# Kernel optimization log

Measured on AMD Instinct MI355X. Metric: run time of the kernel, lower is better.

## Reference

```python
import jax, jax.numpy as jnp
import numpy as np

N, K, C, H, V = 4096, 32, 128, 128, 21   # residues, kNN, node/edge dim, hidden, vocab
NEG_SLOPE = 0.2

def gatv2(src_feat, tgt_feat, edge_feat, Wl, bl, Wr, br, We, be, att, b_out):
    # GATv2Conv (1 head, eval mode) on a regular kNN graph.
    # src_feat: [N,K,Din] gathered source-node features per edge; tgt_feat: [N,Din]
    xl = src_feat @ Wl + bl                       # [N,K,C]
    xr = tgt_feat @ Wr + br                       # [N,C]
    ee = edge_feat @ We + be                      # [N,K,C]
    m = jax.nn.leaky_relu(xl + xr[:, None, :] + ee, NEG_SLOPE)
    alpha = jax.nn.softmax(jnp.einsum('nkc,c->nk', m, att), axis=1)
    return jnp.einsum('nk,nkc->nc', alpha, xl) + b_out

def setup_inputs():
    key = jax.random.key(0)
    ks = jax.random.split(key, 32)
    w = lambda k, s: jax.random.normal(k, s, jnp.float32) * 0.05
    z0 = lambda s: jnp.zeros(s, jnp.float32)
    return dict(
        E=jax.random.normal(ks[0], (N, K, C), jnp.float32),
        E_idx=jax.random.randint(ks[1], (N, K), 0, N),
        S=jax.random.randint(ks[2], (N,), 0, V),
        mask=jnp.ones((N,), jnp.float32),
        chain_M=jnp.ones((N,), jnp.float32),
        z=jax.random.normal(ks[3], (N,), jnp.float32),
        Wl1=w(ks[4], (C, C)), bl1=z0((C,)),
        Wr1=w(ks[5], (C, C)), br1=z0((C,)),
        We1=w(ks[6], (C, C)), be1=z0((C,)),
        a1=w(ks[7], (C,)), bo1=z0((C,)),
        Wl2=w(ks[8], (C + H, C)), bl2=z0((C,)),
        Wr2=w(ks[9], (C + H, C)), br2=z0((C,)),
        We2=w(ks[10], (C, C)), be2=z0((C,)),
        a2=w(ks[11], (C,)), bo2=z0((C,)),
        W_s=w(ks[12], (V, H)),
        W_out=w(ks[13], (C, V)), b_out=z0((V,)),
    )

def reference(E, E_idx, S, mask, chain_M, z,
              Wl1, bl1, Wr1, br1, We1, be1, a1, bo1,
              Wl2, bl2, Wr2, br2, We2, be2, a2, bo2,
              W_s, W_out, b_out):
    # encoder GAT over zero-initialized node features
    x0 = jnp.zeros((N, C), E.dtype)
    node_attr = gatv2(x0[E_idx], x0, E, Wl1, bl1, Wr1, br1, We1, be1, a1, bo1)
    seq_attr = W_s[S]                                        # [N,H]
    h_full = jnp.concatenate([node_attr, seq_attr], -1)      # [N,C+H]
    h_mask = jnp.concatenate([node_attr, jnp.zeros_like(seq_attr)], -1)
    cm = chain_M * mask
    decoding_order = jnp.argsort((cm + 1e-4) * jnp.abs(z))   # [N]
    P = jax.nn.one_hot(decoding_order, N, dtype=E.dtype)     # [N,N] permutation
    L = 1.0 - jnp.triu(jnp.ones((N, N), E.dtype))            # strictly lower tri
    order_mask_backward = jnp.einsum('ij,iq,jp->qp', L, P, P)
    mask_attend = jnp.take_along_axis(order_mask_backward, E_idx, axis=1)[..., None]
    m1d = mask[:, None, None]
    mask_bw = m1d * mask_attend
    mask_fw = m1d * (1.0 - mask_attend)
    # per-edge source features: neighbor seq embedding visible only if decoded earlier
    src = h_full[E_idx] * mask_bw + h_mask[E_idx] * mask_fw  # [N,K,C+H]
    out = gatv2(src, h_mask, E, Wl2, bl2, Wr2, br2, We2, be2, a2, bo2)
    logits = out @ W_out + b_out
    return jax.nn.log_softmax(logits, axis=-1)
```

## Files before the change

kernel.cpp:

```cpp
#include <hip/hip_runtime.h>
#include <hip/hip_bf16.h>

typedef short short8 __attribute__((ext_vector_type(8)));
typedef float float4v __attribute__((ext_vector_type(4)));

#define WS_T   0
#define WS_D   2688
#define WS_C   2816
#define WS_O   2944
#define WS_A2  3072
#define WS_KEY 3200

__device__ __forceinline__ unsigned int pack2bf(float a, float b) {
  union { float f; unsigned int u; } xa, xb;
  xa.f = a; xb.f = b;
  return ((xa.u + 0x8000u) >> 16) | ((xb.u + 0x8000u) & 0xFFFF0000u);
}

__global__ __launch_bounds__(256) void pg7_pre(
    const float* __restrict__ Wl2, const float* __restrict__ Wr2,
    const float* __restrict__ We2, const float* __restrict__ bl1,
    const float* __restrict__ bl2, const float* __restrict__ br2,
    const float* __restrict__ be2, const float* __restrict__ a2,
    const float* __restrict__ bo1, const float* __restrict__ bo2,
    const float* __restrict__ W_s, const float* __restrict__ mask,
    const float* __restrict__ chain_M, const float* __restrict__ z,
    void* __restrict__ ws)
{
  short* wsW = (short*)ws;
  float* F = (float*)ws + 8192;
  const int b = blockIdx.x, tid = threadIdx.x;
  if (b == 0) {
    for (int s = tid; s < 16384; s += 256) {
      const int row = s >> 7, c = s & 127;
      const int q = row >> 5, lh = (row & 31) >> 3, j = row & 7;
      const int t = c >> 4, cl = c & 15;
      union { float f; unsigned int u; } x; x.f = We2[s];
      const unsigned int r = x.u + 0x7FFFu + ((x.u >> 16) & 1u);
      wsW[(((q * 8 + t) * 64) + lh * 16 + cl) * 8 + j] = (short)(r >> 16);
    }
    if (tid < 128) {
      const int c = tid;
      float cl0 = 0.f, cr0 = 0.f;
      for (int i = 0; i < 128; i++) {
        const float s = bl1[i] + bo1[i];
        cl0 += s * Wl2[i * 128 + c];
        cr0 += s * Wr2[i * 128 + c];
      }
      F[WS_D + c]  = be2[c] + bl2[c] + br2[c] + cr0;
      F[WS_C + c]  = cl0;
      F[WS_O + c]  = bl2[c] + bo2[c];
      F[WS_A2 + c] = a2[c];
    }
  } else if (b <= 21) {
    const int v = b - 1;
    if (tid < 128) {
      const int c = tid;
      float acc = 0.f;
      for (int h = 0; h < 128; h++)
        acc += W_s[v * 128 + h] * Wl2[(128 + h) * 128 + c];
      F[WS_T + v * 128 + c] = acc;
    }
  } else {
    const int n = (b - 22) * 256 + tid;
    F[WS_KEY + n] = (chain_M[n] * mask[n] + 1e-4f) * fabsf(z[n]);
  }
}

__global__ __launch_bounds__(256) void pg7_main(
    const float* __restrict__ E, const int* __restrict__ E_idx,
    const int* __restrict__ S, const float* __restrict__ mask,
    const float* __restrict__ W_out, const float* __restrict__ b_out,
    const void* __restrict__ ws, float* __restrict__ out)
{
  __shared__ float ldsout[4][128];
  __shared__ float ldswk[4][32];
  __shared__ int   ldsrv[4][32];

  const short* wsW = (const short*)ws;
  const float* F = (const float*)ws + 8192;
  const int tid  = threadIdx.x;
  const int wave = tid >> 6;
  const int lane = tid & 63;
  const int quad = lane >> 4;
  const int lid  = lane & 15;
  const int n    = blockIdx.x * 4 + wave;
  const float maskn = mask[n];

  if (lane < 32) {
    const int j = E_idx[n * 32 + lane];
    const float keyn = F[WS_KEY + n], kj = F[WS_KEY + j];
    const int before = (kj < keyn) || (kj == keyn && j < n);
    ldswk[wave][lane] = before ? maskn : 0.f;
    ldsrv[wave][lane] = S[j] * 128;
  }
  __builtin_amdgcn_wave_barrier();

  short8 afr[2][4];
#pragma unroll
  for (int g = 0; g < 2; g++) {
    const float* erow = E + (size_t)(n * 32 + g * 16 + lid) * 128 + quad * 8;
#pragma unroll
    for (int q = 0; q < 4; q++) {
      const float4 A = *(const float4*)(erow + q * 32);
      const float4 B = *(const float4*)(erow + q * 32 + 4);
      union { short8 s; unsigned int u[4]; } v;
      v.u[0] = pack2bf(A.x, A.y);
      v.u[1] = pack2bf(A.z, A.w);
      v.u[2] = pack2bf(B.x, B.y);
      v.u[3] = pack2bf(B.z, B.w);
      afr[g][q] = v.s;
    }
  }

  int rows[2][4]; float wks[2][4];
#pragma unroll
  for (int g = 0; g < 2; g++)
#pragma unroll
    for (int r = 0; r < 4; r++) {
      const int kk = g * 16 + quad * 4 + r;
      rows[g][r] = ldsrv[wave][kk];
      wks[g][r]  = ldswk[wave][kk];
    }

  float part[2][4] = {{0.f, 0.f, 0.f, 0.f}, {0.f, 0.f, 0.f, 0.f}};
#pragma unroll
  for (int t = 0; t < 8; t++) {
    short8 bfr[4];
#pragma unroll
    for (int q = 0; q < 4; q++)
      bfr[q] = *(const short8*)(wsW + (((q * 8 + t) * 64) + lane) * 8);
    float4v ac0 = {0.f, 0.f, 0.f, 0.f}, ac1 = {0.f, 0.f, 0.f, 0.f};
#pragma unroll
    for (int q = 0; q < 4; q++) {
      ac0 = __builtin_amdgcn_mfma_f32_16x16x32_bf16(afr[0][q], bfr[q], ac0, 0, 0, 0);
      ac1 = __builtin_amdgcn_mfma_f32_16x16x32_bf16(afr[1][q], bfr[q], ac1, 0, 0, 0);
    }
    const int c = t * 16 + lid;
    const float dvt  = F[WS_D + c] + maskn * F[WS_C + c];
    const float a2vt = F[WS_A2 + c];
#pragma unroll
    for (int r = 0; r < 4; r++) {
      float v0 = ac0[r] + dvt + wks[0][r] * F[WS_T + rows[0][r] + c];
      float v1 = ac1[r] + dvt + wks[1][r] * F[WS_T + rows[1][r] + c];
      v0 = fmaxf(v0, 0.f) + 0.2f * fminf(v0, 0.f);
      v1 = fmaxf(v1, 0.f) + 0.2f * fminf(v1, 0.f);
      part[0][r] = fmaf(v0, a2vt, part[0][r]);
      part[1][r] = fmaf(v1, a2vt, part[1][r]);
    }
  }
  float sreg[2][4];
#pragma unroll
  for (int g = 0; g < 2; g++)
#pragma unroll
    for (int r = 0; r < 4; r++) {
      float v = part[g][r];
      v += __shfl_xor(v, 1);
      v += __shfl_xor(v, 2);
      v += __shfl_xor(v, 4);
      v += __shfl_xor(v, 8);
      sreg[g][r] = v;
    }

  float mx = -1e30f;
#pragma unroll
  for (int g = 0; g < 2; g++)
#pragma unroll
    for (int r = 0; r < 4; r++) mx = fmaxf(mx, sreg[g][r]);
  mx = fmaxf(mx, __shfl_xor(mx, 16));
  mx = fmaxf(mx, __shfl_xor(mx, 32));
  float eg[2][4], esum = 0.f;
#pragma unroll
  for (int g = 0; g < 2; g++)
#pragma unroll
    for (int r = 0; r < 4; r++) {
      eg[g][r] = expf(sreg[g][r] - mx);
      esum += eg[g][r];
    }
  esum += __shfl_xor(esum, 16);
  esum += __shfl_xor(esum, 32);
  const float inv = 1.f / esum;
  float cg[2][4];
#pragma unroll
  for (int g = 0; g < 2; g++)
#pragma unroll
    for (int r = 0; r < 4; r++) cg[g][r] = eg[g][r] * inv * wks[g][r];

  float o0 = F[WS_O + lane]      + maskn * F[WS_C + lane];
  float o1 = F[WS_O + lane + 64] + maskn * F[WS_C + lane + 64];
#pragma unroll
  for (int kk = 0; kk < 32; kk++) {
    const int g = kk >> 4, sq = (kk >> 2) & 3, r = kk & 3;
    const float cf = __shfl(cg[g][r], sq * 16);
    const int row = ldsrv[wave][kk];
    o0 = fmaf(cf, F[WS_T + row + lane], o0);
    o1 = fmaf(cf, F[WS_T + row + lane + 64], o1);
  }
  ldsout[wave][lane]      = o0;
  ldsout[wave][lane + 64] = o1;
  __builtin_amdgcn_wave_barrier();

  float l0 = 0.f, l1 = 0.f, l2 = 0.f, l3 = 0.f;
  if (lane < 21) {
    const float* wo = W_out + lane;
#pragma unroll 8
    for (int c = 0; c < 128; c += 4) {
      l0 = fmaf(ldsout[wave][c],     wo[c * 21],       l0);
      l1 = fmaf(ldsout[wave][c + 1], wo[(c + 1) * 21], l1);
      l2 = fmaf(ldsout[wave][c + 2], wo[(c + 2) * 21], l2);
      l3 = fmaf(ldsout[wave][c + 3], wo[(c + 3) * 21], l3);
    }
  }
  float lg = (lane < 21) ? (b_out[lane] + ((l0 + l1) + (l2 + l3))) : -1e30f;
  float lmx = lg;
  lmx = fmaxf(lmx, __shfl_xor(lmx, 1));
  lmx = fmaxf(lmx, __shfl_xor(lmx, 2));
  lmx = fmaxf(lmx, __shfl_xor(lmx, 4));
  lmx = fmaxf(lmx, __shfl_xor(lmx, 8));
  lmx = fmaxf(lmx, __shfl_xor(lmx, 16));
  float ex = (lane < 21) ? expf(lg - lmx) : 0.f;
  float es = ex;
  es += __shfl_xor(es, 1);
  es += __shfl_xor(es, 2);
  es += __shfl_xor(es, 4);
  es += __shfl_xor(es, 8);
  es += __shfl_xor(es, 16);
  if (lane < 21)
    out[n * 21 + lane] = lg - lmx - logf(es);
}

extern "C" void kernel_launch(void* const* d_in, const int* in_sizes, int n_in,
                              void* d_out, int out_size, void* d_ws, size_t ws_size,
                              hipStream_t stream)
{
  const float* E       = (const float*)d_in[0];
  const int*   E_idx   = (const int*)d_in[1];
  const int*   S       = (const int*)d_in[2];
  const float* mask    = (const float*)d_in[3];
  const float* chain_M = (const float*)d_in[4];
  const float* z       = (const float*)d_in[5];
  const float* bl1     = (const float*)d_in[7];
  const float* bo1     = (const float*)d_in[13];
  const float* Wl2     = (const float*)d_in[14];
  const float* bl2     = (const float*)d_in[15];
  const float* Wr2     = (const float*)d_in[16];
  const float* br2     = (const float*)d_in[17];
  const float* We2     = (const float*)d_in[18];
  const float* be2     = (const float*)d_in[19];
  const float* a2      = (const float*)d_in[20];
  const float* bo2     = (const float*)d_in[21];
  const float* W_s     = (const float*)d_in[22];
  const float* W_out   = (const float*)d_in[23];
  const float* b_out   = (const float*)d_in[24];

  pg7_pre<<<38, 256, 0, stream>>>(Wl2, Wr2, We2, bl1, bl2, br2, be2, a2,
                                  bo1, bo2, W_s, mask, chain_M, z, d_ws);
  pg7_main<<<1024, 256, 0, stream>>>(E, E_idx, S, mask, W_out, b_out, d_ws,
                                     (float*)d_out);
}
```

Before: 173.0 us.

## Fold output projection into per-vocab tables to skip per-node 128-wide aggregation

```diff
diff --git a/kernel.cpp b/kernel.cpp
--- a/kernel.cpp
+++ b/kernel.cpp
@@ -10,6 +10,9 @@
 #define WS_O   2944
 #define WS_A2  3072
 #define WS_KEY 3200
+#define WS_G   7296
+#define WS_B0  7744
+#define WS_B1  7776
 
 __device__ __forceinline__ unsigned int pack2bf(float a, float b) {
   union { float f; unsigned int u; } xa, xb;
@@ -17,7 +20,7 @@
   return ((xa.u + 0x8000u) >> 16) | ((xb.u + 0x8000u) & 0xFFFF0000u);
 }
 
-__global__ __launch_bounds__(256) void pg7_pre(
+__global__ __launch_bounds__(256) void pg8_pre(
     const float* __restrict__ Wl2, const float* __restrict__ Wr2,
     const float* __restrict__ We2, const float* __restrict__ bl1,
     const float* __restrict__ bl2, const float* __restrict__ br2,
@@ -67,13 +70,38 @@
   }
 }
 
-__global__ __launch_bounds__(256) void pg7_main(
+__global__ __launch_bounds__(256) void pg8_pre2(
+    const float* __restrict__ W_out, const float* __restrict__ b_out,
+    void* __restrict__ ws)
+{
+  float* F = (float*)ws + 8192;
+  const int idx = blockIdx.x * 256 + threadIdx.x;
+  if (idx < 441) {
+    const int v = idx / 21, u = idx % 21;
+    float acc = 0.f;
+    for (int c = 0; c < 128; c++)
+      acc += F[WS_T + v * 128 + c] * W_out[c * 21 + u];
+    F[WS_G + v * 21 + u] = acc;
+  } else if (idx < 462) {
+    const int u = idx - 441;
+    float acc = b_out[u];
+    for (int c = 0; c < 128; c++)
+      acc += F[WS_O + c] * W_out[c * 21 + u];
+    F[WS_B0 + u] = acc;
+  } else if (idx < 483) {
+    const int u = idx - 462;
+    float acc = 0.f;
+    for (int c = 0; c < 128; c++)
+      acc += F[WS_C + c] * W_out[c * 21 + u];
+    F[WS_B1 + u] = acc;
+  }
+}
+
+__global__ __launch_bounds__(256, 4) void pg8_main(
     const float* __restrict__ E, const int* __restrict__ E_idx,
     const int* __restrict__ S, const float* __restrict__ mask,
-    const float* __restrict__ W_out, const float* __restrict__ b_out,
     const void* __restrict__ ws, float* __restrict__ out)
 {
-  __shared__ float ldsout[4][128];
   __shared__ float ldswk[4][32];
   __shared__ int   ldsrv[4][32];
 
@@ -92,7 +120,7 @@
     const float keyn = F[WS_KEY + n], kj = F[WS_KEY + j];
     const int before = (kj < keyn) || (kj == keyn && j < n);
     ldswk[wave][lane] = before ? maskn : 0.f;
-    ldsrv[wave][lane] = S[j] * 128;
+    ldsrv[wave][lane] = S[j];
   }
   __builtin_amdgcn_wave_barrier();
 
@@ -119,7 +147,7 @@
 #pragma unroll
     for (int r = 0; r < 4; r++) {
       const int kk = g * 16 + quad * 4 + r;
-      rows[g][r] = ldsrv[wave][kk];
+      rows[g][r] = ldsrv[wave][kk] * 128;
       wks[g][r]  = ldswk[wave][kk];
     }
 
@@ -186,32 +214,15 @@
 #pragma unroll
     for (int r = 0; r < 4; r++) cg[g][r] = eg[g][r] * inv * wks[g][r];
 
-  float o0 = F[WS_O + lane]      + maskn * F[WS_C + lane];
-  float o1 = F[WS_O + lane + 64] + maskn * F[WS_C + lane + 64];
+  float lg = (lane < 21) ? (F[WS_B0 + lane] + maskn * F[WS_B1 + lane]) : -1e30f;
 #pragma unroll
   for (int kk = 0; kk < 32; kk++) {
     const int g = kk >> 4, sq = (kk >> 2) & 3, r = kk & 3;
     const float cf = __shfl(cg[g][r], sq * 16);
-    const int row = ldsrv[wave][kk];
-    o0 = fmaf(cf, F[WS_T + row + lane], o0);
-    o1 = fmaf(cf, F[WS_T + row + lane + 64], o1);
-  }
-  ldsout[wave][lane]      = o0;
-  ldsout[wave][lane + 64] = o1;
-  __builtin_amdgcn_wave_barrier();
-
-  float l0 = 0.f, l1 = 0.f, l2 = 0.f, l3 = 0.f;
-  if (lane < 21) {
-    const float* wo = W_out + lane;
-#pragma unroll 8
-    for (int c = 0; c < 128; c += 4) {
-      l0 = fmaf(ldsout[wave][c],     wo[c * 21],       l0);
-      l1 = fmaf(ldsout[wave][c + 1], wo[(c + 1) * 21], l1);
-      l2 = fmaf(ldsout[wave][c + 2], wo[(c + 2) * 21], l2);
-      l3 = fmaf(ldsout[wave][c + 3], wo[(c + 3) * 21], l3);
-    }
-  }
-  float lg = (lane < 21) ? (b_out[lane] + ((l0 + l1) + (l2 + l3))) : -1e30f;
+    const int row = ldsrv[wave][kk] * 21;
+    if (lane < 21) lg = fmaf(cf, F[WS_G + row + lane], lg);
+  }
+
   float lmx = lg;
   lmx = fmaxf(lmx, __shfl_xor(lmx, 1));
   lmx = fmaxf(lmx, __shfl_xor(lmx, 2));
@@ -253,8 +264,8 @@
   const float* W_out   = (const float*)d_in[23];
   const float* b_out   = (const float*)d_in[24];
 
-  pg7_pre<<<38, 256, 0, stream>>>(Wl2, Wr2, We2, bl1, bl2, br2, be2, a2,
+  pg8_pre<<<38, 256, 0, stream>>>(Wl2, Wr2, We2, bl1, bl2, br2, be2, a2,
                                   bo1, bo2, W_s, mask, chain_M, z, d_ws);
-  pg7_main<<<1024, 256, 0, stream>>>(E, E_idx, S, mask, W_out, b_out, d_ws,
-                                     (float*)d_out);
-}
+  pg8_pre2<<<2, 256, 0, stream>>>(W_out, b_out, d_ws);
+  pg8_main<<<1024, 256, 0, stream>>>(E, E_idx, S, mask, d_ws, (float*)d_out);
+}
```

Result: slower. 181.0 us (+4.6%).
